# Kernel tuning notes

Measured on AMD Instinct MI355X. Metric: run time of the kernel, lower is better.

The kernel has to match this reference:

```python
import jax, jax.numpy as jnp
import numpy as np

DIM = 1024
INTER = 512
E = 16            # n_routed_experts
TOPK = 4          # n_activated_experts
N_GROUPS = 4
TOPK_GROUPS = 2
ROUTE_SCALE = 1.0
INIT_STD = 0.02
B, S = 2, 1024


def setup_inputs() -> dict:
    key = jax.random.key(0)
    ks = jax.random.split(key, 8)
    return {
        "x": jax.random.normal(ks[0], (B, S, DIM), jnp.float32),
        "gate_w": jax.random.normal(ks[1], (E, DIM), jnp.float32) * INIT_STD,
        "gate_bias": jnp.zeros((E,), jnp.float32),
        "w1": jax.random.normal(ks[2], (E, INTER, DIM), jnp.float32) * INIT_STD,
        "w2": jax.random.normal(ks[3], (E, DIM, INTER), jnp.float32) * INIT_STD,
        "w3": jax.random.normal(ks[4], (E, INTER, DIM), jnp.float32) * INIT_STD,
        "ws1": jax.random.normal(ks[5], (INTER, DIM), jnp.float32) * INIT_STD,
        "ws2": jax.random.normal(ks[6], (DIM, INTER), jnp.float32) * INIT_STD,
        "ws3": jax.random.normal(ks[7], (INTER, DIM), jnp.float32) * INIT_STD,
    }


def reference(x, gate_w, gate_bias, w1, w2, w3, ws1, ws2, ws3):
    Bx, Sx, D = x.shape
    T = Bx * Sx
    xf = x.reshape(T, D)

    # ---- Gate: sigmoid scores + expert bias, group-limited top-k ----
    scores = jax.nn.sigmoid(xf @ gate_w.T)          # [T, E]
    original_scores = scores
    s = scores + gate_bias                          # bias only affects selection
    sg = s.reshape(T, N_GROUPS, E // N_GROUPS)
    group_scores = sg.max(axis=-1)                  # [T, G]
    _, gidx = jax.lax.top_k(group_scores, TOPK_GROUPS)
    keep = jnp.zeros((T, N_GROUPS), bool).at[jnp.arange(T)[:, None], gidx].set(True)
    s_masked = jnp.where(keep[:, :, None], sg, -jnp.inf).reshape(T, E)
    _, idx = jax.lax.top_k(s_masked, TOPK)          # [T, topk]
    weights = jnp.take_along_axis(original_scores, idx, axis=1) * ROUTE_SCALE

    # combine weights as sparse [T, E] matrix (scatter of top-k weights)
    comb = jnp.zeros((T, E), x.dtype).at[jnp.arange(T)[:, None], idx].add(weights)

    # ---- Routed experts: SwiGLU per expert, weighted combine ----
    h1 = jnp.einsum('td,eid->tei', xf, w1)          # [T, E, inter]
    h3 = jnp.einsum('td,eid->tei', xf, w3)
    h = jax.nn.silu(h1) * h3
    y = jnp.einsum('tei,edi,te->td', h, w2, comb)   # weighted combine

    # ---- Shared expert (SwiGLU MLP) ----
    z = (jax.nn.silu(xf @ ws1.T) * (xf @ ws3.T)) @ ws2.T

    return (y + z).reshape(Bx, Sx, D)
```

## Files before the change

kernel.cpp:

```cpp
#include <hip/hip_runtime.h>

#define T_TOK  2048
#define DIMD   1024
#define INTERI 512
#define NEXP   16
#define NSEG   17

typedef __bf16 bf16x8 __attribute__((ext_vector_type(8)));
typedef float  f32x4  __attribute__((ext_vector_type(4)));

__device__ __forceinline__ unsigned short f2b(float f) {
    union { float f; unsigned int u; } c; c.f = f;
    unsigned int u = c.u;
    unsigned int r = (u + 0x7FFFu + ((u >> 16) & 1u)) >> 16;
    return (unsigned short)r;
}

__device__ __forceinline__ void cp16(const unsigned short* g, unsigned short* l) {
    __builtin_amdgcn_global_load_lds(
        (const __attribute__((address_space(1))) unsigned int*)g,
        (__attribute__((address_space(3))) unsigned int*)l,
        16, 0, 0);
}

__global__ __launch_bounds__(256) void cvt_all_kernel(
    const float* __restrict__ x,  const float* __restrict__ w1,
    const float* __restrict__ w3, const float* __restrict__ w2,
    const float* __restrict__ ws1, const float* __restrict__ ws3,
    const float* __restrict__ ws2,
    unsigned short* __restrict__ xb,  unsigned short* __restrict__ w1b,
    unsigned short* __restrict__ w3b, unsigned short* __restrict__ w2b,
    unsigned short* __restrict__ ws1b, unsigned short* __restrict__ ws3b,
    unsigned short* __restrict__ ws2b)
{
    int g = blockIdx.x * 256 + threadIdx.x;
    const float* s; unsigned short* d; int i;
    if      (g < 524288)  { s = x;   d = xb;   i = g; }
    else if (g < 2621440) { s = w1;  d = w1b;  i = g - 524288; }
    else if (g < 4718592) { s = w3;  d = w3b;  i = g - 2621440; }
    else if (g < 6815744) { s = w2;  d = w2b;  i = g - 4718592; }
    else if (g < 6946816) { s = ws1; d = ws1b; i = g - 6815744; }
    else if (g < 7077888) { s = ws3; d = ws3b; i = g - 6946816; }
    else                  { s = ws2; d = ws2b; i = g - 7077888; }
    float4 v = ((const float4*)s)[i];
    ushort4 o;
    o.x = f2b(v.x); o.y = f2b(v.y); o.z = f2b(v.z); o.w = f2b(v.w);
    ((ushort4*)d)[i] = o;
}

__global__ __launch_bounds__(256) void gate_score_kernel(
    const float* __restrict__ x, const float* __restrict__ gw,
    const float* __restrict__ gb,
    unsigned* __restrict__ sel, float4* __restrict__ selw)
{
    int tok  = blockIdx.x * 4 + (threadIdx.x >> 6);
    int lane = threadIdx.x & 63;
    const float* xp = x + (size_t)tok * DIMD;
    float xv[16];
#pragma unroll
    for (int j = 0; j < 16; ++j) xv[j] = xp[j * 64 + lane];

    float sc[16];
#pragma unroll
    for (int e = 0; e < 16; ++e) {
        const float* gwe = gw + e * DIMD;
        float p0 = 0.f, p1 = 0.f;
#pragma unroll
        for (int j = 0; j < 16; j += 2) {
            p0 += xv[j]     * gwe[j * 64 + lane];
            p1 += xv[j + 1] * gwe[(j + 1) * 64 + lane];
        }
        float p = p0 + p1;
#pragma unroll
        for (int o = 32; o; o >>= 1) p += __shfl_xor(p, o, 64);
        sc[e] = p;
    }
    if (lane != 0) return;

    float orig[16], s[16];
#pragma unroll
    for (int e = 0; e < 16; ++e) {
        orig[e] = 1.f / (1.f + expf(-sc[e]));
        s[e] = orig[e] + gb[e];
    }
    float gmax[4];
#pragma unroll
    for (int g = 0; g < 4; ++g) {
        float m = s[4 * g];
        for (int j = 1; j < 4; ++j) m = fmaxf(m, s[4 * g + j]);
        gmax[g] = m;
    }
    int g0 = 0;
    for (int g = 1; g < 4; ++g) if (gmax[g] > gmax[g0]) g0 = g;
    int g1 = -1;
    for (int g = 0; g < 4; ++g) { if (g == g0) continue; if (g1 < 0 || gmax[g] > gmax[g1]) g1 = g; }
    unsigned keep = (0xFu << (4 * g0)) | (0xFu << (4 * g1));
    unsigned used = 0;
    unsigned pk = 0;
    float w4[4];
    for (int j = 0; j < 4; ++j) {
        int best = -1;
        for (int e = 0; e < 16; ++e) {
            if (!((keep >> e) & 1u) || ((used >> e) & 1u)) continue;
            if (best < 0 || s[e] > s[best]) best = e;
        }
        used |= 1u << best;
        pk |= ((unsigned)best) << (4 * j);
        w4[j] = orig[best];
    }
    sel[tok] = pk;
    selw[tok] = make_float4(w4[0], w4[1], w4[2], w4[3]);
}

__global__ __launch_bounds__(256) void build_lists_kernel(
    const unsigned* __restrict__ sel, const float4* __restrict__ selw,
    int* __restrict__ counts, int* __restrict__ lst, float* __restrict__ lstw)
{
    const int e    = blockIdx.x;
    const int tid  = threadIdx.x;
    const int wave = tid >> 6;
    const int lane = tid & 63;

    __shared__ int wsum[4];
    __shared__ int basev;
    if (tid == 0) basev = 0;
    __syncthreads();

    for (int c = 0; c < T_TOK / 256; ++c) {
        int t = c * 256 + tid;
        unsigned s = sel[t];
        int match = -1;
#pragma unroll
        for (int j = 0; j < 4; ++j)
            if (((s >> (4 * j)) & 15u) == (unsigned)e) match = j;
        unsigned long long m = __ballot(match >= 0);
        int wpre = __popcll(m & ((1ull << lane) - 1ull));
        if (lane == 0) wsum[wave] = __popcll(m);
        __syncthreads();
        int pre = basev;
        for (int wv = 0; wv < wave; ++wv) pre += wsum[wv];
        if (match >= 0) {
            int pos = pre + wpre;
            lst [e * T_TOK + pos] = t;
            const float* wp = (const float*)&selw[t];
            lstw[e * T_TOK + pos] = wp[match];
        }
        __syncthreads();
        if (tid == 0) basev += wsum[0] + wsum[1] + wsum[2] + wsum[3];
        __syncthreads();
    }
    if (tid == 0) counts[e] = basev;
}

__global__ __launch_bounds__(256, 4) void gemm1_kernel(
    const unsigned short* __restrict__ xb,
    const unsigned short* __restrict__ w1b,
    const unsigned short* __restrict__ w3b,
    const unsigned short* __restrict__ ws1b,
    const unsigned short* __restrict__ ws3b,
    const int* __restrict__ counts,
    const int* __restrict__ lst,
    unsigned short* __restrict__ H)
{
    int b = blockIdx.x;
    int seg, mt, nt;
    if (b < 2048) {
        int xcd = b & 7, slot = b >> 3;
        seg = xcd + 8 * (slot >> 7);
        int tile = slot & 127;
        nt = tile & 3; mt = tile >> 2;
    } else {
        seg = NEXP;
        int tile = b - 2048;
        nt = tile & 3; mt = tile >> 2;
    }
    const int n_e = (seg == NEXP) ? T_TOK : counts[seg];
    const int m0  = mt * 64;
    if (m0 >= n_e) return;
    const int n0  = nt * 128;

    const unsigned short* w1p = (seg == NEXP) ? ws1b : w1b + (size_t)seg * INTERI * DIMD;
    const unsigned short* w3p = (seg == NEXP) ? ws3b : w3b + (size_t)seg * INTERI * DIMD;
    const int* lste = lst + seg * T_TOK;

    __shared__ __align__(16) unsigned short lA [2][64][32];
    __shared__ __align__(16) unsigned short lB1[2][128][32];
    __shared__ __align__(16) unsigned short lB3[2][128][32];

    const int tid  = threadIdx.x;
    const int wave = tid >> 6;
    const int lane = tid & 63;
    const int r4   = tid >> 2;
    const int skg  = (tid & 3) * 8;

    int ra = m0 + r4; if (ra > n_e - 1) ra = n_e - 1;
    int tok = (seg == NEXP) ? ra : lste[ra];
    const unsigned short* gA  = xb  + (size_t)tok * DIMD + skg;
    const unsigned short* gB1a = w1p + (size_t)(n0 + r4) * DIMD + skg;
    const unsigned short* gB1b = w1p + (size_t)(n0 + r4 + 64) * DIMD + skg;
    const unsigned short* gB3a = w3p + (size_t)(n0 + r4) * DIMD + skg;
    const unsigned short* gB3b = w3p + (size_t)(n0 + r4 + 64) * DIMD + skg;

    const int wb = wave * 512;

    f32x4 acc1[2][4], acc3[2][4];
    const f32x4 zero = {0.f, 0.f, 0.f, 0.f};
#pragma unroll
    for (int i = 0; i < 2; ++i)
#pragma unroll
        for (int j = 0; j < 4; ++j) { acc1[i][j] = zero; acc3[i][j] = zero; }

    const int wm   = (wave & 1) * 32;
    const int wn   = (wave >> 1) * 64;
    const int quad = lane >> 4;
    const int lrow = lane & 15;

    for (int k0 = 0; k0 < DIMD; k0 += 64) {
#pragma unroll
        for (int kk = 0; kk < 2; ++kk) {
            cp16(gA   + k0 + kk * 32, &lA [kk][0][0]  + wb);
            cp16(gB1a + k0 + kk * 32, &lB1[kk][0][0]  + wb);
            cp16(gB1b + k0 + kk * 32, &lB1[kk][64][0] + wb);
            cp16(gB3a + k0 + kk * 32, &lB3[kk][0][0]  + wb);
            cp16(gB3b + k0 + kk * 32, &lB3[kk][64][0] + wb);
        }
        __syncthreads();
#pragma unroll
        for (int kk = 0; kk < 2; ++kk) {
            bf16x8 a[2], b1[4], b3[4];
#pragma unroll
            for (int t = 0; t < 2; ++t)
                a[t] = *(const bf16x8*)&lA[kk][wm + t * 16 + lrow][quad * 8];
#pragma unroll
            for (int t = 0; t < 4; ++t) {
                b1[t] = *(const bf16x8*)&lB1[kk][wn + t * 16 + lrow][quad * 8];
                b3[t] = *(const bf16x8*)&lB3[kk][wn + t * 16 + lrow][quad * 8];
            }
#pragma unroll
            for (int i = 0; i < 2; ++i)
#pragma unroll
                for (int j = 0; j < 4; ++j) {
                    acc1[i][j] = __builtin_amdgcn_mfma_f32_16x16x32_bf16(a[i], b1[j], acc1[i][j], 0, 0, 0);
                    acc3[i][j] = __builtin_amdgcn_mfma_f32_16x16x32_bf16(a[i], b3[j], acc3[i][j], 0, 0, 0);
                }
        }
        __syncthreads();
    }

    unsigned short* Hseg = H + (size_t)seg * T_TOK * INTERI;
#pragma unroll
    for (int i = 0; i < 2; ++i) {
        int rbase = m0 + wm + i * 16 + quad * 4;
#pragma unroll
        for (int r = 0; r < 4; ++r) {
            int row = rbase + r;
            if (row >= n_e) continue;
            unsigned short* hrow = Hseg + (size_t)row * INTERI + n0 + wn + lrow;
#pragma unroll
            for (int j = 0; j < 4; ++j) {
                float v1 = acc1[i][j][r];
                float v3 = acc3[i][j][r];
                float hv = (v1 / (1.f + __expf(-v1))) * v3;
                hrow[j * 16] = f2b(hv);
            }
        }
    }
}

__global__ __launch_bounds__(256, 4) void gemm2_kernel(
    const unsigned short* __restrict__ H,
    const unsigned short* __restrict__ w2b,
    const unsigned short* __restrict__ ws2b,
    const int* __restrict__ counts,
    const int* __restrict__ lst,
    const float* __restrict__ lstw,
    float* __restrict__ y)
{
    int b = blockIdx.x;
    int seg, mt, nt;
    if (b < 4096) {
        int xcd = b & 7, slot = b >> 3;
        seg = xcd + 8 * (slot >> 8);
        int tile = slot & 255;
        nt = tile & 7; mt = tile >> 3;
    } else {
        seg = NEXP;
        int tile = b - 4096;
        nt = tile & 7; mt = tile >> 3;
    }
    const int n_e = (seg == NEXP) ? T_TOK : counts[seg];
    const int m0  = mt * 64;
    if (m0 >= n_e) return;
    const int n0  = nt * 128;

    const unsigned short* w2p  = (seg == NEXP) ? ws2b : w2b + (size_t)seg * DIMD * INTERI;
    const unsigned short* Hseg = H + (size_t)seg * T_TOK * INTERI;

    __shared__ __align__(16) unsigned short lA[2][64][32];
    __shared__ __align__(16) unsigned short lB[2][128][32];

    const int tid  = threadIdx.x;
    const int wave = tid >> 6;
    const int lane = tid & 63;
    const int r4   = tid >> 2;
    const int skg  = (tid & 3) * 8;

    int ra = m0 + r4; if (ra > n_e - 1) ra = n_e - 1;
    const unsigned short* gA  = Hseg + (size_t)ra * INTERI + skg;
    const unsigned short* gB0 = w2p + (size_t)(n0 + r4) * INTERI + skg;
    const unsigned short* gB1 = w2p + (size_t)(n0 + r4 + 64) * INTERI + skg;

    const int wb = wave * 512;

    f32x4 acc[2][4];
    const f32x4 zero = {0.f, 0.f, 0.f, 0.f};
#pragma unroll
    for (int i = 0; i < 2; ++i)
#pragma unroll
        for (int j = 0; j < 4; ++j) acc[i][j] = zero;

    const int wm   = (wave & 1) * 32;
    const int wn   = (wave >> 1) * 64;
    const int quad = lane >> 4;
    const int lrow = lane & 15;

    for (int k0 = 0; k0 < INTERI; k0 += 64) {
#pragma unroll
        for (int kk = 0; kk < 2; ++kk) {
            cp16(gA  + k0 + kk * 32, &lA[kk][0][0]  + wb);
            cp16(gB0 + k0 + kk * 32, &lB[kk][0][0]  + wb);
            cp16(gB1 + k0 + kk * 32, &lB[kk][64][0] + wb);
        }
        __syncthreads();
#pragma unroll
        for (int kk = 0; kk < 2; ++kk) {
            bf16x8 a[2], bv[4];
#pragma unroll
            for (int t = 0; t < 2; ++t)
                a[t] = *(const bf16x8*)&lA[kk][wm + t * 16 + lrow][quad * 8];
#pragma unroll
            for (int t = 0; t < 4; ++t)
                bv[t] = *(const bf16x8*)&lB[kk][wn + t * 16 + lrow][quad * 8];
#pragma unroll
            for (int i = 0; i < 2; ++i)
#pragma unroll
                for (int j = 0; j < 4; ++j)
                    acc[i][j] = __builtin_amdgcn_mfma_f32_16x16x32_bf16(a[i], bv[j], acc[i][j], 0, 0, 0);
        }
        __syncthreads();
    }

#pragma unroll
    for (int i = 0; i < 2; ++i) {
        int rbase = m0 + wm + i * 16 + quad * 4;
#pragma unroll
        for (int r = 0; r < 4; ++r) {
            int row = rbase + r;
            if (row >= n_e) continue;
            int tok; float wt;
            if (seg == NEXP) { tok = row; wt = 1.f; }
            else { tok = lst[seg * T_TOK + row]; wt = lstw[seg * T_TOK + row]; }
            float* yrow = y + (size_t)tok * DIMD + n0 + wn + lrow;
#pragma unroll
            for (int j = 0; j < 4; ++j)
                atomicAdd(&yrow[j * 16], wt * acc[i][j][r]);
        }
    }
}

extern "C" void kernel_launch(void* const* d_in, const int* in_sizes, int n_in,
                              void* d_out, int out_size, void* d_ws, size_t ws_size,
                              hipStream_t stream)
{
    const float* x   = (const float*)d_in[0];
    const float* gw  = (const float*)d_in[1];
    const float* gb  = (const float*)d_in[2];
    const float* w1  = (const float*)d_in[3];
    const float* w2  = (const float*)d_in[4];
    const float* w3  = (const float*)d_in[5];
    const float* ws1 = (const float*)d_in[6];
    const float* ws2 = (const float*)d_in[7];
    const float* ws3 = (const float*)d_in[8];

    char* base = (char*)d_ws;
    size_t off = 0;
    auto alloc = [&](size_t bytes) {
        char* q = base + off; off += (bytes + 255) & ~(size_t)255; return q;
    };
    unsigned short* xb   = (unsigned short*)alloc((size_t)T_TOK * DIMD * 2);
    unsigned short* w1b  = (unsigned short*)alloc((size_t)NEXP * INTERI * DIMD * 2);
    unsigned short* w3b  = (unsigned short*)alloc((size_t)NEXP * INTERI * DIMD * 2);
    unsigned short* w2b  = (unsigned short*)alloc((size_t)NEXP * DIMD * INTERI * 2);
    unsigned short* ws1b = (unsigned short*)alloc((size_t)INTERI * DIMD * 2);
    unsigned short* ws3b = (unsigned short*)alloc((size_t)INTERI * DIMD * 2);
    unsigned short* ws2b = (unsigned short*)alloc((size_t)DIMD * INTERI * 2);
    unsigned short* Hb   = (unsigned short*)alloc((size_t)NSEG * T_TOK * INTERI * 2);
    int*            cnts = (int*)alloc(NEXP * 4);
    int*            lstp = (int*)alloc((size_t)NEXP * T_TOK * 4);
    float*          lstw = (float*)alloc((size_t)NEXP * T_TOK * 4);
    unsigned*       selp = (unsigned*)alloc((size_t)T_TOK * 4);
    float4*         selw = (float4*)alloc((size_t)T_TOK * 16);

    hipMemsetAsync(d_out, 0, (size_t)T_TOK * DIMD * 4, stream);

    cvt_all_kernel<<<28160, 256, 0, stream>>>(x, w1, w3, w2, ws1, ws3, ws2,
                                              xb, w1b, w3b, w2b, ws1b, ws3b, ws2b);
    gate_score_kernel<<<T_TOK / 4, 256, 0, stream>>>(x, gw, gb, selp, selw);
    build_lists_kernel<<<NEXP, 256, 0, stream>>>(selp, selw, cnts, lstp, lstw);
    gemm1_kernel<<<2176, 256, 0, stream>>>(xb, w1b, w3b, ws1b, ws3b, cnts, lstp, Hb);
    gemm2_kernel<<<4352, 256, 0, stream>>>(Hb, w2b, ws2b, cnts, lstp, lstw, (float*)d_out);
}
```

Measured before the change: 272.1 us.

## Replace atomic scatter-add with per-slot partial planes and a combine pass

Each token's routing slot index is packed into the upper bits of its expert list entry. GEMM2 then writes its weighted results with plain stores into one of five partial-output planes (four routed slots plus the shared expert) instead of doing float atomicAdd into y. A new combine kernel sums the five planes into the output, which also removes the output memset. This avoids atomic contention, at the cost of an extra 40MB workspace and a read pass over it.

```diff
diff --git a/kernel.cpp b/kernel.cpp
--- a/kernel.cpp
+++ b/kernel.cpp
@@ -141,7 +141,7 @@
         for (int wv = 0; wv < wave; ++wv) pre += wsum[wv];
         if (match >= 0) {
             int pos = pre + wpre;
-            lst [e * T_TOK + pos] = t;
+            lst [e * T_TOK + pos] = t | (match << 16);
             const float* wp = (const float*)&selw[t];
             lstw[e * T_TOK + pos] = wp[match];
         }
@@ -194,7 +194,7 @@
     const int skg  = (tid & 3) * 8;
 
     int ra = m0 + r4; if (ra > n_e - 1) ra = n_e - 1;
-    int tok = (seg == NEXP) ? ra : lste[ra];
+    int tok = (seg == NEXP) ? ra : (lste[ra] & 0xFFFF);
     const unsigned short* gA  = xb  + (size_t)tok * DIMD + skg;
     const unsigned short* gB1a = w1p + (size_t)(n0 + r4) * DIMD + skg;
     const unsigned short* gB1b = w1p + (size_t)(n0 + r4 + 64) * DIMD + skg;
@@ -274,7 +274,7 @@
     const int* __restrict__ counts,
     const int* __restrict__ lst,
     const float* __restrict__ lstw,
-    float* __restrict__ y)
+    float* __restrict__ P)
 {
     int b = blockIdx.x;
     int seg, mt, nt;
@@ -357,15 +357,37 @@
         for (int r = 0; r < 4; ++r) {
             int row = rbase + r;
             if (row >= n_e) continue;
-            int tok; float wt;
-            if (seg == NEXP) { tok = row; wt = 1.f; }
-            else { tok = lst[seg * T_TOK + row]; wt = lstw[seg * T_TOK + row]; }
-            float* yrow = y + (size_t)tok * DIMD + n0 + wn + lrow;
+            int tok, slot; float wt;
+            if (seg == NEXP) { tok = row; slot = 4; wt = 1.f; }
+            else {
+                int ent = lst[seg * T_TOK + row];
+                tok = ent & 0xFFFF; slot = ent >> 16;
+                wt = lstw[seg * T_TOK + row];
+            }
+            float* prow = P + ((size_t)slot * T_TOK + tok) * DIMD + n0 + wn + lrow;
 #pragma unroll
             for (int j = 0; j < 4; ++j)
-                atomicAdd(&yrow[j * 16], wt * acc[i][j][r]);
-        }
-    }
+                prow[j * 16] = wt * acc[i][j][r];
+        }
+    }
+}
+
+__global__ __launch_bounds__(256) void combine_kernel(
+    const float4* __restrict__ P, float4* __restrict__ y)
+{
+    const int i = blockIdx.x * 256 + threadIdx.x;
+    const size_t plane = (size_t)T_TOK * DIMD / 4;
+    float4 a = P[i];
+    float4 b = P[plane + i];
+    float4 c = P[2 * plane + i];
+    float4 d = P[3 * plane + i];
+    float4 e = P[4 * plane + i];
+    float4 o;
+    o.x = a.x + b.x + c.x + d.x + e.x;
+    o.y = a.y + b.y + c.y + d.y + e.y;
+    o.z = a.z + b.z + c.z + d.z + e.z;
+    o.w = a.w + b.w + c.w + d.w + e.w;
+    y[i] = o;
 }
 
 extern "C" void kernel_launch(void* const* d_in, const int* in_sizes, int n_in,
@@ -400,13 +422,13 @@
     float*          lstw = (float*)alloc((size_t)NEXP * T_TOK * 4);
     unsigned*       selp = (unsigned*)alloc((size_t)T_TOK * 4);
     float4*         selw = (float4*)alloc((size_t)T_TOK * 16);
-
-    hipMemsetAsync(d_out, 0, (size_t)T_TOK * DIMD * 4, stream);
+    float*          Pb   = (float*)alloc((size_t)5 * T_TOK * DIMD * 4);
 
     cvt_all_kernel<<<28160, 256, 0, stream>>>(x, w1, w3, w2, ws1, ws3, ws2,
                                               xb, w1b, w3b, w2b, ws1b, ws3b, ws2b);
     gate_score_kernel<<<T_TOK / 4, 256, 0, stream>>>(x, gw, gb, selp, selw);
     build_lists_kernel<<<NEXP, 256, 0, stream>>>(selp, selw, cnts, lstp, lstw);
     gemm1_kernel<<<2176, 256, 0, stream>>>(xb, w1b, w3b, ws1b, ws3b, cnts, lstp, Hb);
-    gemm2_kernel<<<4352, 256, 0, stream>>>(Hb, w2b, ws2b, cnts, lstp, lstw, (float*)d_out);
-}
+    gemm2_kernel<<<4352, 256, 0, stream>>>(Hb, w2b, ws2b, cnts, lstp, lstw, Pb);
+    combine_kernel<<<(T_TOK * DIMD / 4) / 256, 256, 0, stream>>>((const float4*)Pb, (float4*)d_out);
+}
```

After: 257.9 us. 1.05x faster.
